# Optimization experiments

Measured on AMD Instinct MI355X. Metric: run time of the kernel, lower is better.

The kernel has to match this reference:

```python
import jax, jax.numpy as jnp
import numpy as np
from jax import lax

B, T, R, D = 32, 128, 9, 512


def conv2d(x, w, b):
    # x: (N,C,H,W), w: (O,I,kh,kw)
    y = lax.conv_general_dilated(x, w, (1, 1), 'VALID', dimension_numbers=('NCHW', 'OIHW', 'NCHW'))
    return y + b[None, :, None, None]


def pad1(x):
    return jnp.pad(x, ((0, 0), (0, 0), (1, 1), (1, 1)))


def maxpool2(x):
    return lax.reduce_window(x, -jnp.inf, lax.max, (1, 1, 2, 2), (1, 1, 2, 2), 'VALID')


def f2f_similarity(q, t, qm, tm):
    # q,t: (B,T,R,D). Region-pairwise sims then Chamfer: max over target regions p (axis 3), mean over query regions o (axis 2).
    sim = jnp.einsum('biok,bjpk->biopj', q, t)   # (B,T,R,R,T) large intermediate
    sim = jnp.mean(jnp.max(sim, axis=3), axis=2)  # (B,T,T)
    smask = qm[:, :, None] * tm[:, None, :]       # (B,T,T)
    sim = jnp.where(smask > 0, sim, 0.0)
    return sim, smask


def visil_head(sim, mask, w1, b1, w2, b2, w3, b3, wf, bf):
    # ViSiL VideoComperator: zeropad1+conv3x3+relu+maxpool2 (x2), zeropad1+conv3x3+relu, 1x1 conv
    x = sim[:, None]   # (N,1,T,T)
    m = mask[:, None]
    x = maxpool2(jax.nn.relu(conv2d(pad1(x), w1, b1)))
    m = maxpool2(m)
    x = maxpool2(jax.nn.relu(conv2d(pad1(x), w2, b2)))
    m = maxpool2(m)
    x = jax.nn.relu(conv2d(pad1(x), w3, b3))
    x = conv2d(x, wf, bf)   # 1x1 conv -> 1 channel
    return x[:, 0], m[:, 0]


def chamfer_v2v(s, m):
    # masked Chamfer: max over axis 2, masked mean over axis 1
    s = jnp.where(m > 0, s, -jnp.inf)
    s = jnp.max(s, axis=2)
    mm = jnp.max(m, axis=2)
    s = jnp.where(mm > 0, s, 0.0)
    return jnp.sum(s, axis=1) / jnp.sum(mm, axis=1)


def setup_inputs():
    key = jax.random.key(0)
    ks = jax.random.split(key, 8)
    return {
        'anchors': jax.random.normal(ks[0], (B, T, R, D), jnp.float32),
        'positives': jax.random.normal(ks[1], (B, T, R, D), jnp.float32),
        'negatives': jax.random.normal(ks[2], (B, T, R, D), jnp.float32),
        'anchors_masks': jnp.ones((B, T), jnp.float32),
        'positive_masks': jnp.ones((B, T), jnp.float32),
        'negative_masks': jnp.ones((B, T), jnp.float32),
        'w1': jax.random.normal(ks[3], (32, 1, 3, 3), jnp.float32) * 0.05,
        'b1': jnp.zeros((32,), jnp.float32),
        'w2': jax.random.normal(ks[4], (64, 32, 3, 3), jnp.float32) * 0.05,
        'b2': jnp.zeros((64,), jnp.float32),
        'w3': jax.random.normal(ks[5], (128, 64, 3, 3), jnp.float32) * 0.05,
        'b3': jnp.zeros((128,), jnp.float32),
        'wf': jax.random.normal(ks[6], (1, 128, 1, 1), jnp.float32) * 0.05,
        'bf': jnp.zeros((1,), jnp.float32),
    }


def reference(anchors, positives, negatives, anchors_masks, positive_masks, negative_masks, w1, b1, w2, b2, w3, b3, wf, bf):
    pos_sim, pos_mask = f2f_similarity(anchors, positives, anchors_masks, positive_masks)
    neg_sim, neg_mask = f2f_similarity(anchors, negatives, anchors_masks, negative_masks)
    sim = jnp.concatenate([pos_sim, neg_sim], 0)
    smask = jnp.concatenate([pos_mask, neg_mask], 0)
    sim, smask = visil_head(sim, smask, w1, b1, w2, b2, w3, b3, wf, bf)
    # SimilarityRegularizationLoss(min_val=-1, max_val=1)
    loss = jnp.sum(jax.nn.relu(-1.0 - sim)) + jnp.sum(jax.nn.relu(sim - 1.0))
    sim = jnp.clip(sim, -1.0, 1.0)  # Hardtanh
    v2v = chamfer_v2v(sim, smask)   # (2B,)
    pos_pair, neg_pair = jnp.split(v2v[:, None], 2, axis=0)
    return pos_pair, neg_pair, loss
```

## Files before the change

### kernel.cpp

```cpp
#include <hip/hip_runtime.h>
#include <math.h>

#define BTRD (128*9*512)

typedef _Float16 half8 __attribute__((ext_vector_type(8)));
typedef float f32x4 __attribute__((ext_vector_type(4)));

__global__ __launch_bounds__(256) void prep_kernel(
    const float* __restrict__ P, const float* __restrict__ Nn,
    _Float16* __restrict__ Pf, _Float16* __restrict__ Nf,
    const float* __restrict__ w2, const float* __restrict__ w3,
    _Float16* __restrict__ w2t, _Float16* __restrict__ w3t)
{
  int bid = blockIdx.x;
  if (bid < 18432) {
    int which = bid / 9216;
    const float* in = which == 0 ? P : Nn;
    _Float16* out = which == 0 ? Pf : Nf;
    int idx = (bid - which * 9216) * 256 + threadIdx.x;
    const float4* in4 = (const float4*)in;
    float4 a = in4[idx * 2], c = in4[idx * 2 + 1];
    half8 h = { (_Float16)a.x, (_Float16)a.y, (_Float16)a.z, (_Float16)a.w,
                (_Float16)c.x, (_Float16)c.y, (_Float16)c.z, (_Float16)c.w };
    ((half8*)out)[idx] = h;
  } else {
    int idx = (bid - 18432) * 256 + threadIdx.x;
    if (idx < 18432) {
      int tap = idx >> 11, oc = (idx >> 5) & 63, ic = idx & 31;
      w2t[idx] = (_Float16)w2[(oc * 32 + ic) * 9 + tap];
    } else if (idx < 18432 + 73728) {
      int j = idx - 18432;
      int tap = j >> 13, oc = (j >> 6) & 127, ic = j & 63;
      w3t[j] = (_Float16)w3[(oc * 64 + ic) * 9 + tap];
    }
  }
}

template<int O, int OB>
__device__ __forceinline__ void sim_run(
    const float* __restrict__ Q32, const _Float16* __restrict__ TP,
    const _Float16* __restrict__ TN,
    _Float16* __restrict__ lds, int i0, int tid, int jq, int b,
    const float* __restrict__ qm, const float* __restrict__ pm,
    const float* __restrict__ nm, float* __restrict__ simout)
{
  int lane = tid & 63;
  int lrow = lane & 15, lk8 = lane >> 4;
  _Float16* tb0 = lds + 73728;
  _Float16* tb1 = lds + 73728 + 4096;

  {
    const float* qb = Q32 + ((size_t)(i0 * 9) << 9);
#pragma unroll
    for (int it = 0; it < 18; it++) {
      int c = it * 512 + tid;
      int r = c >> 6, sp = c & 63;
      const float* src = qb + ((size_t)r << 9) + (sp << 3);
      float4 a = *(const float4*)src;
      float4 cc = *(const float4*)(src + 4);
      half8 h = { (_Float16)a.x, (_Float16)a.y, (_Float16)a.z, (_Float16)a.w,
                  (_Float16)cc.x, (_Float16)cc.y, (_Float16)cc.z, (_Float16)cc.w };
      *(half8*)&lds[r * 512 + ((sp ^ (r & 7)) << 3)] = h;
    }
  }
  __syncthreads();

  int jc = tid >> 2, spc = tid & 3;
  int ld = jc * 32 + ((spc ^ ((jc >> 1) & 3)) << 3);

  float* ex = (float*)(lds + 73728);
  const float* qmv = qm + b * 128;
  const float inv9 = 1.0f / 9.0f;

  for (int tsel = 0; tsel < 2; ++tsel) {
    const _Float16* tg = (tsel ? TN : TP) + (size_t)jc * 4608 + (spc << 3);

    half8 st[4];
    f32x4 acc[O][2], mx[O][2];
#pragma unroll
    for (int oo = 0; oo < O; oo++)
#pragma unroll
      for (int jt = 0; jt < 2; jt++) {
        acc[oo][jt] = (f32x4){0.f, 0.f, 0.f, 0.f};
        mx[oo][jt] = (f32x4){-INFINITY, -INFINITY, -INFINITY, -INFINITY};
      }

#define T_ISSUE(SET, S) do {                                              \
      int _s = (S);                                                       \
      int _p = _s >> 4; if (_p > 8) _p = 8;                               \
      st[SET] = *(const half8*)(tg + (_p << 9) + ((_s & 15) << 5));       \
    } while (0)

#define T_WRITE(SET, PAR) do {                                            \
      _Float16* _b = (PAR) ? tb1 : tb0;                                   \
      *(half8*)&_b[ld] = st[SET];                                         \
    } while (0)

    T_ISSUE(0, 0);
    T_ISSUE(1, 1);
    T_ISSUE(2, 2);
    T_WRITE(0, 0);
    asm volatile("s_waitcnt lgkmcnt(0)" ::: "memory");
    __builtin_amdgcn_s_barrier();
    __builtin_amdgcn_sched_barrier(0);

    for (int p = 0; p < 9; ++p) {
#pragma unroll
      for (int kc = 0; kc < 16; ++kc) {
        int s = p * 16 + kc;
        T_ISSUE((kc + 3) & 3, s + 3);
        T_WRITE((kc + 1) & 3, (kc + 1) & 1);

        const _Float16* cur = (kc & 1) ? tb1 : tb0;
        half8 bfr[2];
#pragma unroll
        for (int jt = 0; jt < 2; jt++) {
          int j = jq * 32 + jt * 16 + lrow;
          bfr[jt] = *(const half8*)&cur[j * 32 + ((lk8 ^ ((j >> 1) & 3)) << 3)];
        }
#pragma unroll
        for (int oo = 0; oo < O; ++oo) {
          int r = lrow * 9 + OB + oo;
          half8 afr = *(const half8*)&lds[r * 512 + ((((kc << 2) + lk8) ^ (r & 7)) << 3)];
          acc[oo][0] = __builtin_amdgcn_mfma_f32_16x16x32_f16(afr, bfr[0], acc[oo][0], 0, 0, 0);
          acc[oo][1] = __builtin_amdgcn_mfma_f32_16x16x32_f16(afr, bfr[1], acc[oo][1], 0, 0, 0);
        }

        if (kc == 15) {
#pragma unroll
          for (int oo = 0; oo < O; oo++)
#pragma unroll
            for (int jt = 0; jt < 2; jt++) {
#pragma unroll
              for (int e = 0; e < 4; e++)
                mx[oo][jt][e] = fmaxf(mx[oo][jt][e], acc[oo][jt][e]);
              acc[oo][jt] = (f32x4){0.f, 0.f, 0.f, 0.f};
            }
        }
        asm volatile("s_waitcnt lgkmcnt(0)" ::: "memory");
        __builtin_amdgcn_s_barrier();
        __builtin_amdgcn_sched_barrier(0);
      }
    }
#undef T_ISSUE
#undef T_WRITE

    f32x4 ps[2];
#pragma unroll
    for (int jt = 0; jt < 2; jt++) {
      ps[jt] = mx[0][jt];
#pragma unroll
      for (int oo = 1; oo < O; oo++) ps[jt] += mx[oo][jt];
    }

    if (OB != 0) {
#pragma unroll
      for (int jt = 0; jt < 2; jt++)
        *(f32x4*)&ex[((jq * 64 + lane) * 2 + jt) * 4] = ps[jt];
    }
    __syncthreads();
    if (OB == 0) {
      const float* tm = (tsel ? nm : pm) + b * 128;
      int pb = b + tsel * 32;
#pragma unroll
      for (int jt = 0; jt < 2; jt++) {
        ps[jt] += *(const f32x4*)&ex[((jq * 64 + lane) * 2 + jt) * 4];
        int j = jq * 32 + jt * 16 + lrow;
        float tmv = tm[j];
#pragma unroll
        for (int e = 0; e < 4; e++) {
          int i = i0 + (lk8 << 2) + e;
          float m = qmv[i] * tmv;
          simout[((size_t)pb << 14) + (i << 7) + j] = (m > 0.f) ? ps[jt][e] * inv9 : 0.f;
        }
      }
    }
    __syncthreads();
  }
}

__global__ __launch_bounds__(512, 1) void sim_mfma_kernel(
    const float* __restrict__ A32, const _Float16* __restrict__ Pf,
    const _Float16* __restrict__ Nf,
    const float* __restrict__ qm, const float* __restrict__ pm,
    const float* __restrict__ nm, float* __restrict__ simout)
{
  __shared__ _Float16 lds[81920];

  int n = blockIdx.x;
  int xcd = n & 7, slot = n >> 3;
  int b = xcd * 4 + (slot >> 3);
  int ib = slot & 7;
  const float* Q32 = A32 + (size_t)b * BTRD;
  const _Float16* TP = Pf + (size_t)b * BTRD;
  const _Float16* TN = Nf + (size_t)b * BTRD;
  int i0 = ib * 16;

  int tid = threadIdx.x;
  int w = tid >> 6;
  int jq = w & 3;
  if ((w >> 2) == 0)
    sim_run<5, 0>(Q32, TP, TN, lds, i0, tid, jq, b, qm, pm, nm, simout);
  else
    sim_run<4, 5>(Q32, TP, TN, lds, i0, tid, jq, b, qm, pm, nm, simout);
}

__global__ __launch_bounds__(256) void conv1_kernel(
    const float* __restrict__ sim, const float* __restrict__ w1,
    const float* __restrict__ b1, _Float16* __restrict__ x1)
{
  __shared__ float w_s[288];
  __shared__ float b_s[32];
  int tid = threadIdx.x;
  for (int e = tid; e < 288; e += 256) w_s[e] = w1[e];
  if (tid < 32) b_s[tid] = b1[tid];
  __syncthreads();

  int idx = blockIdx.x * 256 + tid;
  int x = idx & 63, y = (idx >> 6) & 63, b2 = idx >> 12;
  const float* sb = sim + (size_t)b2 * 16384;

  float patch[4][4];
#pragma unroll
  for (int r = 0; r < 4; r++) {
    int Y = 2 * y - 1 + r;
#pragma unroll
    for (int c = 0; c < 4; c++) {
      int X = 2 * x - 1 + c;
      patch[r][c] = (Y >= 0 && Y < 128 && X >= 0 && X < 128) ? sb[Y * 128 + X] : 0.f;
    }
  }

  _Float16 vout[32];
#pragma unroll
  for (int oc = 0; oc < 32; oc++) {
    float c00 = 0, c01 = 0, c10 = 0, c11 = 0;
#pragma unroll
    for (int tap = 0; tap < 9; tap++) {
      int dy = tap / 3, dx = tap - dy * 3;
      float w = w_s[oc * 9 + tap];
      c00 = fmaf(w, patch[dy][dx], c00);
      c01 = fmaf(w, patch[dy][dx + 1], c01);
      c10 = fmaf(w, patch[dy + 1][dx], c10);
      c11 = fmaf(w, patch[dy + 1][dx + 1], c11);
    }
    float v = fmaxf(fmaxf(c00, c01), fmaxf(c10, c11)) + b_s[oc];
    vout[oc] = (_Float16)fmaxf(v, 0.f);
  }
  _Float16* dst = x1 + (((size_t)b2 * 64 + y) * 64 + x) * 32;
#pragma unroll
  for (int q = 0; q < 4; q++)
    *(half8*)(dst + q * 8) = *(half8*)&vout[q * 8];
}

__global__ __launch_bounds__(256, 2) void conv2_mfma(
    const _Float16* __restrict__ x1, const _Float16* __restrict__ w2t,
    const float* __restrict__ bb, _Float16* __restrict__ x2)
{
  __shared__ _Float16 in_s[4 * 6 * 66 * 8];
  __shared__ _Float16 w_s[9 * 64 * 40];
  __shared__ _Float16 pool_s[4][32 * 32];

  int b2 = blockIdx.y, ystrip = blockIdx.x;
  int y0 = ystrip * 4;
  int tid = threadIdx.x;
  int w = tid >> 6, lane = tid & 63;
  int wyp = w >> 1, wn = w & 1;
  int lrow = lane & 15, lk8 = lane >> 4;

  {
    int px = tid >> 2, seg = tid & 3;
    const _Float16* base = x1 + ((size_t)b2 * 64) * 64 * 32;
    for (int rr = 0; rr < 6; rr++) {
      int yy = y0 - 1 + rr;
      half8 v = {};
      if (yy >= 0 && yy < 64) v = *(const half8*)(base + ((size_t)yy * 64 + px) * 32 + seg * 8);
      *(half8*)&in_s[((seg * 6 + rr) * 66 + px + 1) * 8] = v;
    }
    if (tid < 48) {
      int pr = tid >> 1, side = tid & 1;
      *(half8*)&in_s[(pr * 66 + side * 65) * 8] = (half8){};
    }
  }
  for (int e = tid; e < 2304; e += 256)
    *(half8*)&w_s[(e >> 2) * 40 + (e & 3) * 8] = *(const half8*)&w2t[e * 8];
  __syncthreads();

  f32x4 acc[2][4][2];
#pragma unroll
  for (int yr = 0; yr < 2; yr++)
#pragma unroll
    for (int xt = 0; xt < 4; xt++)
#pragma unroll
      for (int nt = 0; nt < 2; nt++)
        acc[yr][xt][nt] = (f32x4){0.f, 0.f, 0.f, 0.f};

#pragma unroll
  for (int tap = 0; tap < 9; tap++) {
    int dy = tap / 3, dx = tap - dy * 3;
    half8 bfr[2];
#pragma unroll
    for (int nt = 0; nt < 2; nt++)
      bfr[nt] = *(const half8*)&w_s[(tap * 64 + wn * 32 + nt * 16 + lrow) * 40 + lk8 * 8];
#pragma unroll
    for (int yr = 0; yr < 2; yr++) {
      int rr = 2 * wyp + yr + dy;
#pragma unroll
      for (int xt = 0; xt < 4; xt++) {
        half8 afr = *(const half8*)&in_s[((lk8 * 6 + rr) * 66 + xt * 16 + lrow + dx) * 8];
#pragma unroll
        for (int nt = 0; nt < 2; nt++)
          acc[yr][xt][nt] = __builtin_amdgcn_mfma_f32_16x16x32_f16(afr, bfr[nt], acc[yr][xt][nt], 0, 0, 0);
      }
    }
  }

  float bbv[2] = { bb[wn * 32 + lrow], bb[wn * 32 + 16 + lrow] };
#pragma unroll
  for (int nt = 0; nt < 2; nt++)
#pragma unroll
    for (int xt = 0; xt < 4; xt++)
#pragma unroll
      for (int pe = 0; pe < 2; pe++) {
        float m = fmaxf(fmaxf(acc[0][xt][nt][2 * pe], acc[0][xt][nt][2 * pe + 1]),
                        fmaxf(acc[1][xt][nt][2 * pe], acc[1][xt][nt][2 * pe + 1]));
        float v = fmaxf(m + bbv[nt], 0.f);
        int px = xt * 8 + lk8 * 2 + pe;
        pool_s[w][px * 32 + nt * 16 + lrow] = (_Float16)v;
      }
  __syncthreads();

  {
    int py = ystrip * 2 + wyp;
    int px = lane & 31, half = lane >> 5;
    const _Float16* srcp = &pool_s[w][px * 32 + half * 16];
    _Float16* dst = x2 + (((size_t)b2 * 32 + py) * 32 + px) * 64 + wn * 32 + half * 16;
    *(half8*)dst = *(const half8*)srcp;
    *(half8*)(dst + 8) = *(const half8*)(srcp + 8);
  }
}

__global__ __launch_bounds__(256, 2) void conv3_mfma(
    const _Float16* __restrict__ x2, const _Float16* __restrict__ w3t,
    const float* __restrict__ b3, const float* __restrict__ wf,
    const float* __restrict__ bf, float* __restrict__ shead)
{
  __shared__ _Float16 in_s[8 * 6 * 34 * 8];
  __shared__ _Float16 w_s[9 * 32 * 72];

  int b2 = blockIdx.y, ystrip = blockIdx.x;
  int y0 = ystrip * 4;
  int tid = threadIdx.x, w = tid >> 6, lane = tid & 63;
  int lrow = lane & 15, lk8 = lane >> 4;

  {
    int px = tid >> 3, seg = tid & 7;
    const _Float16* base = x2 + ((size_t)b2 * 32) * 32 * 64;
    for (int rr = 0; rr < 6; rr++) {
      int yy = y0 - 1 + rr;
      half8 v = {};
      if (yy >= 0 && yy < 32) v = *(const half8*)(base + ((size_t)yy * 32 + px) * 64 + seg * 8);
      *(half8*)&in_s[((seg * 6 + rr) * 34 + px + 1) * 8] = v;
    }
    if (tid < 96) {
      int pr = tid >> 1, side = tid & 1;
      *(half8*)&in_s[(pr * 34 + side * 33) * 8] = (half8){};
    }
  }

  f32x4 spart[2];
  spart[0] = (f32x4){0.f, 0.f, 0.f, 0.f};
  spart[1] = (f32x4){0.f, 0.f, 0.f, 0.f};
  int y = y0 + w;

  for (int og = 0; og < 4; og++) {
    __syncthreads();
    for (int e = tid; e < 2304; e += 256) {
      int s = e & 7, o = (e >> 3) & 31, tap = e >> 8;
      *(half8*)&w_s[(tap * 32 + o) * 72 + s * 8] =
          *(const half8*)&w3t[((size_t)(tap * 128 + og * 32 + o)) * 64 + s * 8];
    }
    __syncthreads();

    f32x4 acc[2][2];
#pragma unroll
    for (int mt = 0; mt < 2; mt++)
#pragma unroll
      for (int nt = 0; nt < 2; nt++)
        acc[mt][nt] = (f32x4){0.f, 0.f, 0.f, 0.f};

#pragma unroll
    for (int tap = 0; tap < 9; tap++) {
      int dy = tap / 3, dx = tap - dy * 3;
#pragma unroll
      for (int kc = 0; kc < 2; kc++) {
        half8 bfr[2];
#pragma unroll
        for (int nt = 0; nt < 2; nt++)
          bfr[nt] = *(const half8*)&w_s[(tap * 32 + nt * 16 + lrow) * 72 + kc * 32 + lk8 * 8];
#pragma unroll
        for (int mt = 0; mt < 2; mt++) {
          half8 afr = *(const half8*)&in_s[(((kc * 4 + lk8) * 6 + w + dy) * 34 + mt * 16 + lrow + dx) * 8];
#pragma unroll
          for (int nt = 0; nt < 2; nt++)
            acc[mt][nt] = __builtin_amdgcn_mfma_f32_16x16x32_f16(afr, bfr[nt], acc[mt][nt], 0, 0, 0);
        }
      }
    }

#pragma unroll
    for (int nt = 0; nt < 2; nt++) {
      int oc = og * 32 + nt * 16 + lrow;
      float b3v = b3[oc], wfv = wf[oc];
#pragma unroll
      for (int mt = 0; mt < 2; mt++)
#pragma unroll
        for (int e = 0; e < 4; e++)
          spart[mt][e] = fmaf(fmaxf(acc[mt][nt][e] + b3v, 0.f), wfv, spart[mt][e]);
    }
  }

#pragma unroll
  for (int mt = 0; mt < 2; mt++)
#pragma unroll
    for (int e = 0; e < 4; e++) {
      float v = spart[mt][e];
      v += __shfl_xor(v, 1); v += __shfl_xor(v, 2);
      v += __shfl_xor(v, 4); v += __shfl_xor(v, 8);
      spart[mt][e] = v;
    }
  if (lrow == 0) {
    float bfv = bf[0];
#pragma unroll
    for (int mt = 0; mt < 2; mt++)
#pragma unroll
      for (int e = 0; e < 4; e++) {
        int x = mt * 16 + lk8 * 4 + e;
        shead[(size_t)b2 * 1024 + y * 32 + x] = spart[mt][e] + bfv;
      }
  }
}

__global__ __launch_bounds__(256) void head_final_kernel(
    const float* __restrict__ shead, const float* __restrict__ qm,
    const float* __restrict__ pm, const float* __restrict__ nm,
    float* __restrict__ out, float* __restrict__ loss_ws)
{
  int b2 = blockIdx.x, b = b2 & 31, g = b2 >> 5;
  const float* qmv = qm + b * 128;
  const float* tmv = (g ? nm : pm) + b * 128;

  __shared__ float mq4[32], mt4[32];
  __shared__ float red[256];
  __shared__ float rowv[32], rowm[32];

  int tid = threadIdx.x;
  if (tid < 32) {
    float a = qmv[tid * 4];
    a = fmaxf(a, qmv[tid * 4 + 1]); a = fmaxf(a, qmv[tid * 4 + 2]); a = fmaxf(a, qmv[tid * 4 + 3]);
    mq4[tid] = a;
    float c = tmv[tid * 4];
    c = fmaxf(c, tmv[tid * 4 + 1]); c = fmaxf(c, tmv[tid * 4 + 2]); c = fmaxf(c, tmv[tid * 4 + 3]);
    mt4[tid] = c;
  }
  __syncthreads();

  const float* s = shead + (size_t)b2 * 1024;
  float lp = 0.f;
#pragma unroll
  for (int r = 0; r < 4; r++) {
    float v = s[tid + 256 * r];
    lp += fmaxf(-1.f - v, 0.f) + fmaxf(v - 1.f, 0.f);
  }
  red[tid] = lp;
  __syncthreads();
  for (int off = 128; off; off >>= 1) {
    if (tid < off) red[tid] += red[tid + off];
    __syncthreads();
  }
  if (tid == 0) loss_ws[b2] = red[0];

  if (tid < 32) {
    int y = tid;
    float mqy = mq4[y];
    float rmax = -INFINITY, mm = 0.f;
    for (int x = 0; x < 32; x++) {
      float m = mqy * mt4[x];
      mm = fmaxf(mm, m);
      float v = s[y * 32 + x];
      v = fminf(fmaxf(v, -1.f), 1.f);
      rmax = fmaxf(rmax, m > 0.f ? v : -INFINITY);
    }
    rowv[y] = (mm > 0.f) ? rmax : 0.f;
    rowm[y] = mm;
  }
  __syncthreads();
  if (tid == 0) {
    float ss = 0.f, sm = 0.f;
    for (int y = 0; y < 32; y++) { ss += rowv[y]; sm += rowm[y]; }
    out[b2] = ss / sm;
  }
}

__global__ void loss_sum_kernel(const float* __restrict__ loss_ws, float* __restrict__ out)
{
  float v = loss_ws[threadIdx.x];
#pragma unroll
  for (int off = 32; off >= 1; off >>= 1) v += __shfl_down(v, off);
  if (threadIdx.x == 0) out[64] = v;
}

extern "C" void kernel_launch(void* const* d_in, const int* in_sizes, int n_in,
                              void* d_out, int out_size, void* d_ws, size_t ws_size,
                              hipStream_t stream)
{
  (void)in_sizes; (void)n_in; (void)out_size; (void)ws_size;
  const float* A   = (const float*)d_in[0];
  const float* P   = (const float*)d_in[1];
  const float* Nn  = (const float*)d_in[2];
  const float* qm  = (const float*)d_in[3];
  const float* pm  = (const float*)d_in[4];
  const float* nm  = (const float*)d_in[5];
  const float* w1  = (const float*)d_in[6];
  const float* b1  = (const float*)d_in[7];
  const float* w2  = (const float*)d_in[8];
  const float* b2w = (const float*)d_in[9];
  const float* w3  = (const float*)d_in[10];
  const float* b3  = (const float*)d_in[11];
  const float* wf  = (const float*)d_in[12];
  const float* bf  = (const float*)d_in[13];
  float* out = (float*)d_out;

  const size_t F16SZ = (size_t)BTRD * 32 * sizeof(_Float16);
  char* ws = (char*)d_ws;
  _Float16* Pf = (_Float16*)(ws);
  _Float16* Nf = (_Float16*)(ws + F16SZ);
  char* ws2 = ws + 2 * F16SZ;
  float*     sim   = (float*)(ws2);
  _Float16*  x1    = (_Float16*)(ws2 + (4u << 20));
  _Float16*  x2    = (_Float16*)(ws2 + (20u << 20));
  float*     shead = (float*)(ws2 + (28u << 20));
  _Float16*  w2t   = (_Float16*)(ws2 + (29u << 20));
  _Float16*  w3t   = (_Float16*)(ws2 + (29u << 20) + (256u << 10));
  float*     lws   = (float*)(ws2 + (30u << 20));

  prep_kernel<<<18792, 256, 0, stream>>>(P, Nn, Pf, Nf, w2, w3, w2t, w3t);

  sim_mfma_kernel<<<256, 512, 0, stream>>>(A, Pf, Nf, qm, pm, nm, sim);
  conv1_kernel<<<1024, 256, 0, stream>>>(sim, w1, b1, x1);
  conv2_mfma<<<dim3(16, 64), 256, 0, stream>>>(x1, w2t, b2w, x2);
  conv3_mfma<<<dim3(8, 64), 256, 0, stream>>>(x2, w3t, b3, wf, bf, shead);
  head_final_kernel<<<64, 256, 0, stream>>>(shead, qm, pm, nm, out, lws);
  loss_sum_kernel<<<1, 64, 0, stream>>>(lws, out);
}
```

Measured before the change: 202.1 us.

## Double K-step per barrier and keep ninth query region in registers

The target staging now moves 64 halfs of K per pipeline step instead of 32, which halves the number of LDS barriers per region sweep. Each barrier is followed by two MFMA K-substeps. Query rows 0-7 of each frame stay in LDS (now 64K halfs), while the ninth region is preloaded straight into registers for the warp group whose OB is non-zero, so LDS use drops. The cost is higher register pressure from the 16 half8 fragments and the doubled staging registers, which may lower occupancy.

```diff
diff --git a/kernel.cpp b/kernel.cpp
--- a/kernel.cpp
+++ b/kernel.cpp
@@ -46,21 +46,30 @@
 {
   int lane = tid & 63;
   int lrow = lane & 15, lk8 = lane >> 4;
-  _Float16* tb0 = lds + 73728;
-  _Float16* tb1 = lds + 73728 + 4096;
-
-  {
-    const float* qb = Q32 + ((size_t)(i0 * 9) << 9);
-#pragma unroll
-    for (int it = 0; it < 18; it++) {
-      int c = it * 512 + tid;
-      int r = c >> 6, sp = c & 63;
-      const float* src = qb + ((size_t)r << 9) + (sp << 3);
-      float4 a = *(const float4*)src;
-      float4 cc = *(const float4*)(src + 4);
-      half8 h = { (_Float16)a.x, (_Float16)a.y, (_Float16)a.z, (_Float16)a.w,
-                  (_Float16)cc.x, (_Float16)cc.y, (_Float16)cc.z, (_Float16)cc.w };
-      *(half8*)&lds[r * 512 + ((sp ^ (r & 7)) << 3)] = h;
+
+  const float* qb = Q32 + ((size_t)(i0 * 9) << 9);
+
+#pragma unroll
+  for (int it = 0; it < 16; it++) {
+    int c = it * 512 + tid;
+    int r = c >> 6, sp = c & 63;
+    const float* src = qb + ((size_t)((r >> 3) * 9 + (r & 7)) << 9) + (sp << 3);
+    float4 a = *(const float4*)src;
+    float4 cc = *(const float4*)(src + 4);
+    half8 h = { (_Float16)a.x, (_Float16)a.y, (_Float16)a.z, (_Float16)a.w,
+                (_Float16)cc.x, (_Float16)cc.y, (_Float16)cc.z, (_Float16)cc.w };
+    *(half8*)&lds[r * 512 + ((sp ^ (r & 7)) << 3)] = h;
+  }
+
+  half8 o8f[16];
+  if (OB != 0) {
+    const float* o8src = qb + ((size_t)(lrow * 9 + 8) << 9) + (lk8 << 3);
+#pragma unroll
+    for (int c = 0; c < 16; c++) {
+      float4 a = *(const float4*)(o8src + (c << 5));
+      float4 cc = *(const float4*)(o8src + (c << 5) + 4);
+      o8f[c] = (half8){ (_Float16)a.x, (_Float16)a.y, (_Float16)a.z, (_Float16)a.w,
+                        (_Float16)cc.x, (_Float16)cc.y, (_Float16)cc.z, (_Float16)cc.w };
     }
   }
   __syncthreads();
@@ -68,14 +77,14 @@
   int jc = tid >> 2, spc = tid & 3;
   int ld = jc * 32 + ((spc ^ ((jc >> 1) & 3)) << 3);
 
-  float* ex = (float*)(lds + 73728);
+  float* ex = (float*)(lds + 65536);
   const float* qmv = qm + b * 128;
   const float inv9 = 1.0f / 9.0f;
 
   for (int tsel = 0; tsel < 2; ++tsel) {
     const _Float16* tg = (tsel ? TN : TP) + (size_t)jc * 4608 + (spc << 3);
 
-    half8 st[4];
+    half8 st[4][2];
     f32x4 acc[O][2], mx[O][2];
 #pragma unroll
     for (int oo = 0; oo < O; oo++)
@@ -87,13 +96,16 @@
 
 #define T_ISSUE(SET, S) do {                                              \
       int _s = (S);                                                       \
-      int _p = _s >> 4; if (_p > 8) _p = 8;                               \
-      st[SET] = *(const half8*)(tg + (_p << 9) + ((_s & 15) << 5));       \
+      int _p = _s >> 3; if (_p > 8) _p = 8;                               \
+      const _Float16* _a = tg + (_p << 9) + ((_s & 7) << 6);              \
+      st[SET][0] = *(const half8*)_a;                                     \
+      st[SET][1] = *(const half8*)(_a + 32);                              \
     } while (0)
 
 #define T_WRITE(SET, PAR) do {                                            \
-      _Float16* _b = (PAR) ? tb1 : tb0;                                   \
-      *(half8*)&_b[ld] = st[SET];                                         \
+      _Float16* _b = lds + 65536 + (PAR) * 8192;                          \
+      *(half8*)&_b[ld] = st[SET][0];                                      \
+      *(half8*)&_b[4096 + ld] = st[SET][1];                               \
     } while (0)
 
     T_ISSUE(0, 0);
@@ -106,27 +118,37 @@
 
     for (int p = 0; p < 9; ++p) {
 #pragma unroll
-      for (int kc = 0; kc < 16; ++kc) {
-        int s = p * 16 + kc;
+      for (int kc = 0; kc < 8; ++kc) {
+        int s = p * 8 + kc;
         T_ISSUE((kc + 3) & 3, s + 3);
         T_WRITE((kc + 1) & 3, (kc + 1) & 1);
 
-        const _Float16* cur = (kc & 1) ? tb1 : tb0;
-        half8 bfr[2];
-#pragma unroll
-        for (int jt = 0; jt < 2; jt++) {
-          int j = jq * 32 + jt * 16 + lrow;
-          bfr[jt] = *(const half8*)&cur[j * 32 + ((lk8 ^ ((j >> 1) & 3)) << 3)];
+        const _Float16* buf = lds + 65536 + (kc & 1) * 8192;
+#pragma unroll
+        for (int kh = 0; kh < 2; ++kh) {
+          const _Float16* cur = buf + kh * 4096;
+          int kc32 = (kc << 1) + kh;
+          half8 bfr[2];
+#pragma unroll
+          for (int jt = 0; jt < 2; jt++) {
+            int j = jq * 32 + jt * 16 + lrow;
+            bfr[jt] = *(const half8*)&cur[j * 32 + ((lk8 ^ ((j >> 1) & 3)) << 3)];
+          }
+#pragma unroll
+          for (int oo = 0; oo < O; ++oo) {
+            half8 afr;
+            if (OB + oo == 8) {
+              afr = o8f[kc32];
+            } else {
+              int r = lrow * 8 + OB + oo;
+              afr = *(const half8*)&lds[r * 512 + ((((kc32 << 2) + lk8) ^ (r & 7)) << 3)];
+            }
+            acc[oo][0] = __builtin_amdgcn_mfma_f32_16x16x32_f16(afr, bfr[0], acc[oo][0], 0, 0, 0);
+            acc[oo][1] = __builtin_amdgcn_mfma_f32_16x16x32_f16(afr, bfr[1], acc[oo][1], 0, 0, 0);
+          }
         }
-#pragma unroll
-        for (int oo = 0; oo < O; ++oo) {
-          int r = lrow * 9 + OB + oo;
-          half8 afr = *(const half8*)&lds[r * 512 + ((((kc << 2) + lk8) ^ (r & 7)) << 3)];
-          acc[oo][0] = __builtin_amdgcn_mfma_f32_16x16x32_f16(afr, bfr[0], acc[oo][0], 0, 0, 0);
-          acc[oo][1] = __builtin_amdgcn_mfma_f32_16x16x32_f16(afr, bfr[1], acc[oo][1], 0, 0, 0);
-        }
-
-        if (kc == 15) {
+
+        if (kc == 7) {
 #pragma unroll
           for (int oo = 0; oo < O; oo++)
 #pragma unroll
```

Measured after the change: 273.6 us. +35.4%, slower.
